# Kernel tuning notes

Hardware: AMD Instinct MI355X
Metric: run time of the kernel (lower is better)

The kernel has to match this reference:

```python
import jax, jax.numpy as jnp
import numpy as np

DIM, HEADS = 128, 8
DH = DIM // HEADS
SCALE = DH ** -0.5
N, E = 50000, 800000


def setup_inputs() -> dict:
    key = jax.random.key(0)
    ks = jax.random.split(key, 12)
    w = lambda k: jax.random.normal(k, (DIM, DIM), dtype=jnp.float32) * 0.02
    b = lambda k: jax.random.normal(k, (DIM,), dtype=jnp.float32) * 0.02
    return {
        "q_nodes": jax.random.normal(ks[0], (N, DIM), dtype=jnp.float32),
        "k_edges": jax.random.normal(ks[1], (E, DIM), dtype=jnp.float32),
        "v_edges": jax.random.normal(ks[2], (E, DIM), dtype=jnp.float32),
        "edge_index": jax.random.randint(ks[3], (2, E), 0, N, dtype=jnp.int64),
        "Wq": w(ks[4]), "bq": b(ks[5]),
        "Wk": w(ks[6]), "bk": b(ks[7]),
        "Wv": w(ks[8]), "bv": b(ks[9]),
        "Wo": w(ks[10]), "bo": b(ks[11]),
    }


def reference(q_nodes, k_edges, v_edges, edge_index, Wq, bq, Wk, bk, Wv, bv, Wo, bo):
    n, e = q_nodes.shape[0], k_edges.shape[0]
    dst = edge_index[0]  # src (edge_index[1]) is unused by the module
    q = (q_nodes @ Wq.T + bq).reshape(n, HEADS, DH)
    k = (k_edges @ Wk.T + bk).reshape(e, HEADS, DH)
    v = (v_edges @ Wv.T + bv).reshape(e, HEADS, DH)
    # per-edge score: dot(q[dst], k) per head -> [E, H]
    score = jnp.einsum('ehd,ehd->eh', q[dst], k) * SCALE
    # segment (per-dst-node) softmax over edges, numerically stable
    m = jax.ops.segment_max(score, dst, num_segments=n)          # [N, H]
    ex = jnp.exp(score - m[dst])                                  # [E, H]
    s = jax.ops.segment_sum(ex, dst, num_segments=n)             # [N, H]
    w = ex / (s[dst] + 1e-16)                                     # [E, H]
    weighted_v = (v * w[..., None]).reshape(e, DIM)               # [E, dim]
    aggr = jax.ops.segment_sum(weighted_v, dst, num_segments=n)  # [N, dim]
    return aggr @ Wo.T + bo
```

## Files before the change

### kernel.cpp

```cpp
#include <hip/hip_runtime.h>

#define TM 64
#define NTHREADS 256
#define PAD 132

typedef __attribute__((ext_vector_type(8))) short short8;
typedef __attribute__((ext_vector_type(4))) float f32x4;

__device__ __forceinline__ short f2bf(float f) {
  union { float f; unsigned u; } uf; uf.f = f;
  unsigned r = uf.u + 0x7FFFu + ((uf.u >> 16) & 1u);
  return (short)(r >> 16);
}
__device__ __forceinline__ float bf2f(short s) {
  union { unsigned u; float f; } uf; uf.u = ((unsigned)(unsigned short)s) << 16;
  return uf.f;
}
__device__ __forceinline__ short8 pack8(float4 a, float4 b) {
  short8 r;
  r[0] = f2bf(a.x); r[1] = f2bf(a.y); r[2] = f2bf(a.z); r[3] = f2bf(a.w);
  r[4] = f2bf(b.x); r[5] = f2bf(b.y); r[6] = f2bf(b.z); r[7] = f2bf(b.w);
  return r;
}


__global__ __launch_bounds__(512) void proj_mfma(
    const float* __restrict__ X, const short* __restrict__ Wb,
    const float* __restrict__ bias, float* __restrict__ Y, int M, float scale) {
  __shared__ short Xb[8192];
  int t = threadIdx.x;
  int w = t >> 6, l = t & 63, g = l >> 4, c = l & 15;
  short8 wf[4];
#pragma unroll
  for (int kc = 0; kc < 4; ++kc)
    wf[kc] = *(const short8*)(Wb + (w * 16 + c) * 128 + kc * 32 + g * 8);
  float4 b4 = *(const float4*)(bias + w * 16 + g * 4);

  for (int rb = blockIdx.x * 64; rb < M; rb += gridDim.x * 64) {
    {
      int r = t >> 3, q8 = t & 7;
      int row = rb + r; if (row >= M) row = M - 1;
      const float4* xs = (const float4*)(X + (size_t)row * 128 + q8 * 16);
      float4 x0 = xs[0], x1 = xs[1], x2 = xs[2], x3 = xs[3];
      int sw = (r & 7) << 4;
      *(short8*)((char*)Xb + r * 256 + ((q8 * 32) ^ sw)) = pack8(x0, x1);
      *(short8*)((char*)Xb + r * 256 + ((q8 * 32 + 16) ^ sw)) = pack8(x2, x3);
    }
    __syncthreads();
#pragma unroll
    for (int et = 0; et < 4; ++et) {
      int rl = et * 16 + c;
      f32x4 acc = {};
      int sw = (rl & 7) << 4;
#pragma unroll
      for (int kc = 0; kc < 4; ++kc) {
        short8 xb = *(const short8*)((char*)Xb + rl * 256 + ((kc * 64 + g * 16) ^ sw));
        acc = __builtin_amdgcn_mfma_f32_16x16x32_bf16(wf[kc], xb, acc, 0, 0, 0);
      }
      int row = rb + rl;
      if (row < M) {
        float4 o;
        o.x = (acc[0] + b4.x) * scale; o.y = (acc[1] + b4.y) * scale;
        o.z = (acc[2] + b4.z) * scale; o.w = (acc[3] + b4.w) * scale;
        *(float4*)(Y + (size_t)row * 128 + w * 16 + g * 4) = o;
      }
    }
    __syncthreads();
  }
}


__global__ __launch_bounds__(512) void proj_mfma_h(
    const float* __restrict__ X, const short* __restrict__ Wb,
    const float* __restrict__ bias, short* __restrict__ Yh, int M, float scale) {
  __shared__ short Xb[8192];
  int t = threadIdx.x;
  int w = t >> 6, l = t & 63, g = l >> 4, c = l & 15;
  short8 wf[4];
#pragma unroll
  for (int kc = 0; kc < 4; ++kc)
    wf[kc] = *(const short8*)(Wb + (w * 16 + c) * 128 + kc * 32 + g * 8);
  float4 b4 = *(const float4*)(bias + w * 16 + g * 4);

  for (int rb = blockIdx.x * 64; rb < M; rb += gridDim.x * 64) {
    {
      int r = t >> 3, q8 = t & 7;
      int row = rb + r; if (row >= M) row = M - 1;
      const float4* xs = (const float4*)(X + (size_t)row * 128 + q8 * 16);
      float4 x0 = xs[0], x1 = xs[1], x2 = xs[2], x3 = xs[3];
      int sw = (r & 7) << 4;
      *(short8*)((char*)Xb + r * 256 + ((q8 * 32) ^ sw)) = pack8(x0, x1);
      *(short8*)((char*)Xb + r * 256 + ((q8 * 32 + 16) ^ sw)) = pack8(x2, x3);
    }
    __syncthreads();
#pragma unroll
    for (int et = 0; et < 4; ++et) {
      int rl = et * 16 + c;
      f32x4 acc = {};
      int sw = (rl & 7) << 4;
#pragma unroll
      for (int kc = 0; kc < 4; ++kc) {
        short8 xb = *(const short8*)((char*)Xb + rl * 256 + ((kc * 64 + g * 16) ^ sw));
        acc = __builtin_amdgcn_mfma_f32_16x16x32_bf16(wf[kc], xb, acc, 0, 0, 0);
      }
      int row = rb + rl;
      if (row < M) {
        short4 o;
        o.x = f2bf((acc[0] + b4.x) * scale); o.y = f2bf((acc[1] + b4.y) * scale);
        o.z = f2bf((acc[2] + b4.z) * scale); o.w = f2bf((acc[3] + b4.w) * scale);
        *(short4*)(Yh + (size_t)row * 128 + w * 16 + g * 4) = o;
      }
    }
    __syncthreads();
  }
}


__global__ __launch_bounds__(256) void hist_kernel(const int* __restrict__ dst,
                                                   int* __restrict__ cnt, int E) {
  int e = blockIdx.x * 256 + threadIdx.x;
  if (e < E) atomicAdd(&cnt[dst[e]], 1);
}

__global__ __launch_bounds__(1024) void scan_part(const int* __restrict__ cnt,
                                                  int* __restrict__ part, int N) {
  __shared__ int ws[16];
  int t = threadIdx.x, i = blockIdx.x * 1024 + t;
  int v = (i < N) ? cnt[i] : 0;
#pragma unroll
  for (int d = 1; d < 64; d <<= 1) v += __shfl_xor(v, d);
  if ((t & 63) == 0) ws[t >> 6] = v;
  __syncthreads();
  if (t < 16) {
    int x = ws[t];
#pragma unroll
    for (int d = 1; d < 16; d <<= 1) x += __shfl_xor(x, d);
    if (t == 0) part[blockIdx.x] = x;
  }
}

__global__ __launch_bounds__(64) void scan_offs(int* __restrict__ part, int P) {
  int t = threadIdx.x;
  int carry = 0;
  for (int base = 0; base < P; base += 64) {
    int i = base + t;
    int v = (i < P) ? part[i] : 0;
    int x = v;
#pragma unroll
    for (int d = 1; d < 64; d <<= 1) { int y = __shfl_up(x, d); if (t >= d) x += y; }
    if (i < P) part[i] = x - v + carry;
    carry += __shfl(x, 63);
  }
}

__global__ __launch_bounds__(1024) void scan_final(const int* __restrict__ cnt,
                                                   const int* __restrict__ part,
                                                   int* __restrict__ rp,
                                                   int* __restrict__ cur, int N) {
  __shared__ int ws[16];
  __shared__ int wofs[16];
  int t = threadIdx.x, i = blockIdx.x * 1024 + t;
  int lane = t & 63, wid = t >> 6;
  int v = (i < N) ? cnt[i] : 0;
  int x = v;
#pragma unroll
  for (int d = 1; d < 64; d <<= 1) { int y = __shfl_up(x, d); if (lane >= d) x += y; }
  if (lane == 63) ws[wid] = x;
  __syncthreads();
  if (t == 0) {
    int s = 0;
#pragma unroll
    for (int k2 = 0; k2 < 16; ++k2) { int tmp = ws[k2]; wofs[k2] = s; s += tmp; }
  }
  __syncthreads();
  int incl = x + wofs[wid] + part[blockIdx.x];
  int excl = incl - v;
  if (i < N) {
    rp[i] = excl; cur[i] = excl;
    if (i == N - 1) rp[N] = incl;
  }
}

__global__ __launch_bounds__(256) void perm_kernel(const int* __restrict__ dst,
                                                   int* __restrict__ cursor,
                                                   int* __restrict__ perm, int E) {
  int e = blockIdx.x * 256 + threadIdx.x;
  if (e < E) perm[e] = atomicAdd(&cursor[dst[e]], 1);
}

__global__ __launch_bounds__(256) void wprep4(
    const float* __restrict__ Wq, const float* __restrict__ Wk,
    const float* __restrict__ Wv, const float* __restrict__ Wo,
    short* __restrict__ wqb, short* __restrict__ wkb,
    short* __restrict__ wvb, short* __restrict__ wob) {
  int i = blockIdx.x * 256 + threadIdx.x;
  if (i < 16384) {
    wqb[i] = f2bf(Wq[i]); wkb[i] = f2bf(Wk[i]);
    wvb[i] = f2bf(Wv[i]); wob[i] = f2bf(Wo[i]);
  }
}


__global__ __launch_bounds__(512) void edge_mfma9(
    const float* __restrict__ K, const float* __restrict__ V,
    const int* __restrict__ eidx, const int* __restrict__ perm,
    const short* __restrict__ wkb, const short* __restrict__ wvb,
    const float* __restrict__ bk, const short* __restrict__ qpb,
    float* __restrict__ exb, short* __restrict__ wv, int E) {
  __shared__ short Kb[8192];
  __shared__ short Vb[8192];
  __shared__ int sh_perm[64];
  int t = threadIdx.x;
  int w = t >> 6, l = t & 63, g = l >> 4, c = l & 15;
  float4 bk4 = *(const float4*)(bk + w * 16 + g * 4);
  const short* wkp = wkb + (w * 16 + c) * 128 + g * 8;
  const short* wvp = wvb + (w * 16 + c) * 128 + g * 8;
  const short* qpp = qpb + (size_t)(w * 16 + g * 4);

  int r = t >> 3, q8 = t & 7;
  int b0 = r * 256 + ((q8 * 32) ^ ((r & 7) << 4));
  int stride = gridDim.x * 64;
  int eb = blockIdx.x * 64;

  float4 k0, k1, k2, k3, v0, v1, v2, v3;
  short4 qvb[4];
  int prm_r;
  {
    int row0 = eb + r; if (row0 >= E) row0 = E - 1;
    const float4* ks = (const float4*)(K + (size_t)row0 * 128 + q8 * 16);
    k0 = ks[0]; k1 = ks[1]; k2 = ks[2]; k3 = ks[3];
    const float4* vs = (const float4*)(V + (size_t)row0 * 128 + q8 * 16);
    v0 = vs[0]; v1 = vs[1]; v2 = vs[2]; v3 = vs[3];
    prm_r = perm[row0];
#pragma unroll
    for (int et = 0; et < 4; ++et) {
      int e = eb + et * 16 + c; if (e >= E) e = E - 1;
      qvb[et] = *(const short4*)(qpp + (size_t)eidx[e] * 128);
    }
  }

  for (; eb < E; eb += stride) {
    int ebn = eb + stride;
    bool hn = ebn < E;

    __syncthreads();
    *(short8*)((char*)Kb + b0) = pack8(k0, k1);
    *(short8*)((char*)Kb + (b0 ^ 16)) = pack8(k2, k3);
    *(short8*)((char*)Vb + b0) = pack8(v0, v1);
    *(short8*)((char*)Vb + (b0 ^ 16)) = pack8(v2, v3);
    if (q8 == 0) sh_perm[r] = prm_r;
    __syncthreads();

    short8 wK[4];
#pragma unroll
    for (int kc = 0; kc < 4; ++kc)
      wK[kc] = *(const short8*)(wkp + kc * 32);

    short4 qvn[4];
    int prm_rn = 0;
    if (hn) {
      int rowk = ebn + r; if (rowk >= E) rowk = E - 1;
      const float4* ks = (const float4*)(K + (size_t)rowk * 128 + q8 * 16);
      k0 = ks[0]; k1 = ks[1]; k2 = ks[2]; k3 = ks[3];
      const float4* vs = (const float4*)(V + (size_t)rowk * 128 + q8 * 16);
      v0 = vs[0]; v1 = vs[1]; v2 = vs[2]; v3 = vs[3];
      prm_rn = perm[rowk];
#pragma unroll
      for (int et = 0; et < 4; ++et) {
        int e = ebn + et * 16 + c; if (e >= E) e = E - 1;
        qvn[et] = *(const short4*)(qpp + (size_t)eidx[e] * 128);
      }
    }

    float ex[4];
    int sl[4];
#pragma unroll
    for (int et = 0; et < 4; ++et) {
      int eloc = et * 16 + c;
      int swr = (eloc & 7) << 4;
      sl[et] = sh_perm[eloc];
      f32x4 acc = {};
#pragma unroll
      for (int kc = 0; kc < 4; ++kc) {
        short8 xb = *(const short8*)((char*)Kb + eloc * 256 + ((kc * 64 + g * 16) ^ swr));
        acc = __builtin_amdgcn_mfma_f32_16x16x32_bf16(wK[kc], xb, acc, 0, 0, 0);
      }
      float s = (acc[0] + bk4.x) * bf2f(qvb[et].x) + (acc[1] + bk4.y) * bf2f(qvb[et].y) +
                (acc[2] + bk4.z) * bf2f(qvb[et].z) + (acc[3] + bk4.w) * bf2f(qvb[et].w);
      s += __shfl_xor(s, 16);
      s += __shfl_xor(s, 32);
      ex[et] = __expf(s);
      if (g == 0) exb[(size_t)sl[et] * 8 + w] = ex[et];
    }

    short8 wV[4];
#pragma unroll
    for (int kc = 0; kc < 4; ++kc)
      wV[kc] = *(const short8*)(wvp + kc * 32);

#pragma unroll
    for (int et = 0; et < 4; ++et) {
      int eloc = et * 16 + c;
      int swr = (eloc & 7) << 4;
      f32x4 acc = {};
#pragma unroll
      for (int kc = 0; kc < 4; ++kc) {
        short8 xb = *(const short8*)((char*)Vb + eloc * 256 + ((kc * 64 + g * 16) ^ swr));
        acc = __builtin_amdgcn_mfma_f32_16x16x32_bf16(wV[kc], xb, acc, 0, 0, 0);
      }
      short4 sv;
      sv.x = f2bf(acc[0] * ex[et]); sv.y = f2bf(acc[1] * ex[et]);
      sv.z = f2bf(acc[2] * ex[et]); sv.w = f2bf(acc[3] * ex[et]);
      *(short4*)(wv + (size_t)sl[et] * 128 + w * 16 + g * 4) = sv;
    }

#pragma unroll
    for (int et = 0; et < 4; ++et) qvb[et] = qvn[et];
    prm_r = prm_rn;
  }
}


__global__ __launch_bounds__(256) void pull3(
    const short* __restrict__ wv, const float* __restrict__ exb,
    const int* __restrict__ rp, const float* __restrict__ bv,
    float* __restrict__ aggr, int N) {
  int w = threadIdx.x >> 6, l = threadIdx.x & 63;
  int n = blockIdx.x * 4 + w;
  if (n >= N) return;
  int beg = rp[n], end = rp[n + 1];
  int h = l >> 3;
  float a0 = 0.f, a1 = 0.f, s = 0.f;
  int j = beg;
  for (; j + 1 < end; j += 2) {
    unsigned u0 = *(const unsigned*)(wv + (size_t)j * 128 + l * 2);
    unsigned u1 = *(const unsigned*)(wv + (size_t)(j + 1) * 128 + l * 2);
    float s0 = exb[(size_t)j * 8 + h], s1 = exb[(size_t)(j + 1) * 8 + h];
    a0 += bf2f((short)(u0 & 0xFFFFu)) + bf2f((short)(u1 & 0xFFFFu));
    a1 += bf2f((short)(u0 >> 16)) + bf2f((short)(u1 >> 16));
    s += s0 + s1;
  }
  if (j < end) {
    unsigned u0 = *(const unsigned*)(wv + (size_t)j * 128 + l * 2);
    s += exb[(size_t)j * 8 + h];
    a0 += bf2f((short)(u0 & 0xFFFFu));
    a1 += bf2f((short)(u0 >> 16));
  }
  float2 o;
  if (end > beg) {
    float inv = 1.f / (s + 1e-16f);
    float2 bvv = *(const float2*)(bv + l * 2);
    o.x = a0 * inv + bvv.x; o.y = a1 * inv + bvv.y;
  } else {
    o.x = 0.f; o.y = 0.f;
  }
  *(float2*)(aggr + (size_t)n * 128 + l * 2) = o;
}


__device__ __forceinline__ void stage_x(float (*Xs)[PAD], const float* __restrict__ X,
                                        int rowbase, int M, int t) {
#pragma unroll
  for (int i = 0; i < 8; ++i) {
    int idx = t + NTHREADS * i;
    int r = idx >> 5, q = idx & 31;
    int row = rowbase + r;
    if (row >= M) row = M - 1;
    const float4 v = *(const float4*)(X + (size_t)row * 128 + q * 4);
    *(float4*)(&Xs[r][q * 4]) = v;
  }
}

__device__ __forceinline__ void gemm_tile(const float (*Xs)[PAD], float (*WT)[PAD],
                                          const float* __restrict__ W,
                                          float acc[8][4], int r0, int c0, int t) {
#pragma unroll 1
  for (int kk = 0; kk < 128; kk += 32) {
    {
      int j = t >> 1, half = t & 1;
      const float* src = W + j * 128 + kk + half * 16;
      float4 a = *(const float4*)(src);
      float4 b = *(const float4*)(src + 4);
      float4 c = *(const float4*)(src + 8);
      float4 d = *(const float4*)(src + 12);
      int cb = half * 16;
      WT[cb + 0][j] = a.x;  WT[cb + 1][j] = a.y;  WT[cb + 2][j] = a.z;  WT[cb + 3][j] = a.w;
      WT[cb + 4][j] = b.x;  WT[cb + 5][j] = b.y;  WT[cb + 6][j] = b.z;  WT[cb + 7][j] = b.w;
      WT[cb + 8][j] = c.x;  WT[cb + 9][j] = c.y;  WT[cb + 10][j] = c.z; WT[cb + 11][j] = c.w;
      WT[cb + 12][j] = d.x; WT[cb + 13][j] = d.y; WT[cb + 14][j] = d.z; WT[cb + 15][j] = d.w;
    }
    __syncthreads();
#pragma unroll
    for (int c2 = 0; c2 < 16; ++c2) {
      float4 wa = *(const float4*)(&WT[2 * c2][c0]);
      float4 wb = *(const float4*)(&WT[2 * c2 + 1][c0]);
#pragma unroll
      for (int i = 0; i < 8; ++i) {
        float2 xv = *(const float2*)(&Xs[r0 + i][kk + 2 * c2]);
        acc[i][0] = fmaf(xv.x, wa.x, acc[i][0]);
        acc[i][1] = fmaf(xv.x, wa.y, acc[i][1]);
        acc[i][2] = fmaf(xv.x, wa.z, acc[i][2]);
        acc[i][3] = fmaf(xv.x, wa.w, acc[i][3]);
        acc[i][0] = fmaf(xv.y, wb.x, acc[i][0]);
        acc[i][1] = fmaf(xv.y, wb.y, acc[i][1]);
        acc[i][2] = fmaf(xv.y, wb.z, acc[i][2]);
        acc[i][3] = fmaf(xv.y, wb.w, acc[i][3]);
      }
    }
    __syncthreads();
  }
}

__global__ __launch_bounds__(NTHREADS) void proj_kernel(
    const float* __restrict__ X, const float* __restrict__ W,
    const float* __restrict__ b, float* __restrict__ Y, int M) {
  __shared__ float Xs[TM][PAD];
  __shared__ float WT[32][PAD];
  int t = threadIdx.x;
  int B0 = blockIdx.x * TM;
  stage_x(Xs, X, B0, M, t);
  __syncthreads();
  int r0 = (t >> 5) * 8, m = t & 31, c0 = m * 4;
  float acc[8][4] = {};
  gemm_tile(Xs, WT, W, acc, r0, c0, t);
  float4 bv = ((const float4*)b)[m];
#pragma unroll
  for (int i = 0; i < 8; ++i) {
    int row = B0 + r0 + i;
    if (row < M) {
      float4 o;
      o.x = acc[i][0] + bv.x; o.y = acc[i][1] + bv.y;
      o.z = acc[i][2] + bv.z; o.w = acc[i][3] + bv.w;
      *(float4*)(Y + (size_t)row * 128 + c0) = o;
    }
  }
}

__global__ __launch_bounds__(NTHREADS) void edge_kernel(
    const float* __restrict__ Kin, const float* __restrict__ Vin,
    const int* __restrict__ eidx,
    const float* __restrict__ Wk, const float* __restrict__ bk,
    const float* __restrict__ Wv, const float* __restrict__ bv,
    const float* __restrict__ qp, float* __restrict__ s_sum,
    float* __restrict__ aggr, int E) {
  __shared__ float Xs[TM][PAD];
  __shared__ float WT[32][PAD];
  __shared__ int dsts[TM];
  int t = threadIdx.x;
  int e0 = blockIdx.x * TM;
  if (t < TM) {
    int idx = e0 + t;
    if (idx >= E) idx = E - 1;
    dsts[t] = eidx[idx];
  }
  stage_x(Xs, Kin, e0, E, t);
  __syncthreads();
  int r0 = (t >> 5) * 8, m = t & 31, c0 = m * 4;
  int h = m >> 2;
  float acc[8][4] = {};
  gemm_tile(Xs, WT, Wk, acc, r0, c0, t);
  float4 bkv = ((const float4*)bk)[m];
  float ex[8];
#pragma unroll
  for (int i = 0; i < 8; ++i) {
    int r = r0 + i;
    const float4 qv = *(const float4*)(qp + (size_t)dsts[r] * 128 + c0);
    float p = (acc[i][0] + bkv.x) * qv.x + (acc[i][1] + bkv.y) * qv.y +
              (acc[i][2] + bkv.z) * qv.z + (acc[i][3] + bkv.w) * qv.w;
    p += __shfl_xor(p, 1);
    p += __shfl_xor(p, 2);
    float e = __expf(p * 0.25f);
    ex[i] = e;
    if ((m & 3) == 0 && (e0 + r) < E)
      atomicAdd(&s_sum[(size_t)dsts[r] * 8 + h], e);
  }
  __syncthreads();
  stage_x(Xs, Vin, e0, E, t);
  __syncthreads();
#pragma unroll
  for (int i = 0; i < 8; ++i)
#pragma unroll
    for (int j = 0; j < 4; ++j) acc[i][j] = 0.f;
  gemm_tile(Xs, WT, Wv, acc, r0, c0, t);
  float4 bvv = ((const float4*)bv)[m];
#pragma unroll
  for (int i = 0; i < 8; ++i) {
    int r = r0 + i;
    if ((e0 + r) < E) {
      size_t base = (size_t)dsts[r] * 128 + c0;
      atomicAdd(&aggr[base + 0], (acc[i][0] + bvv.x) * ex[i]);
      atomicAdd(&aggr[base + 1], (acc[i][1] + bvv.y) * ex[i]);
      atomicAdd(&aggr[base + 2], (acc[i][2] + bvv.z) * ex[i]);
      atomicAdd(&aggr[base + 3], (acc[i][3] + bvv.w) * ex[i]);
    }
  }
}

__global__ __launch_bounds__(NTHREADS) void out_kernel(
    const float* __restrict__ aggr, const float* __restrict__ s_sum,
    const float* __restrict__ W, const float* __restrict__ b,
    float* __restrict__ Y, int M) {
  __shared__ float Xs[TM][PAD];
  __shared__ float WT[32][PAD];
  int t = threadIdx.x;
  int B0 = blockIdx.x * TM;
#pragma unroll
  for (int i = 0; i < 8; ++i) {
    int idx = t + NTHREADS * i;
    int r = idx >> 5, q = idx & 31;
    int row = B0 + r;
    if (row >= M) row = M - 1;
    float4 v = *(const float4*)(aggr + (size_t)row * 128 + q * 4);
    float inv = 1.0f / (s_sum[(size_t)row * 8 + (q >> 2)] + 1e-16f);
    v.x *= inv; v.y *= inv; v.z *= inv; v.w *= inv;
    *(float4*)(&Xs[r][q * 4]) = v;
  }
  __syncthreads();
  int r0 = (t >> 5) * 8, m = t & 31, c0 = m * 4;
  float acc[8][4] = {};
  gemm_tile(Xs, WT, W, acc, r0, c0, t);
  float4 bv = ((const float4*)b)[m];
#pragma unroll
  for (int i = 0; i < 8; ++i) {
    int row = B0 + r0 + i;
    if (row < M) {
      float4 o;
      o.x = acc[i][0] + bv.x; o.y = acc[i][1] + bv.y;
      o.z = acc[i][2] + bv.z; o.w = acc[i][3] + bv.w;
      *(float4*)(Y + (size_t)row * 128 + c0) = o;
    }
  }
}


extern "C" void kernel_launch(void* const* d_in, const int* in_sizes, int n_in,
                              void* d_out, int out_size, void* d_ws, size_t ws_size,
                              hipStream_t stream) {
  const float* q_nodes = (const float*)d_in[0];
  const float* k_edges = (const float*)d_in[1];
  const float* v_edges = (const float*)d_in[2];
  const int* eidx = (const int*)d_in[3];
  const float* Wq = (const float*)d_in[4];
  const float* bq = (const float*)d_in[5];
  const float* Wk = (const float*)d_in[6];
  const float* bk = (const float*)d_in[7];
  const float* Wv = (const float*)d_in[8];
  const float* bv = (const float*)d_in[9];
  const float* Wo = (const float*)d_in[10];
  const float* bo = (const float*)d_in[11];

  int N = in_sizes[0] / 128;
  int E = in_sizes[1] / 128;
  int P = (N + 1023) / 1024;

  size_t off = 0;
  auto alloc = [&](size_t b) { size_t o = off; off += (b + 255) & ~(size_t)255; return o; };
  size_t o_qpb  = alloc((size_t)N * 128 * 2);
  size_t o_aggr = alloc((size_t)N * 128 * 4);
  size_t o_exb  = alloc((size_t)E * 8 * 4);
  size_t o_rp   = alloc(((size_t)N + 1) * 4);
  size_t o_cur  = alloc((size_t)N * 4);
  size_t o_cnt  = alloc((size_t)N * 4);
  size_t o_perm = alloc((size_t)E * 4);
  size_t o_part = alloc((size_t)(P + 1) * 4);
  size_t o_wqb  = alloc((size_t)16384 * 2);
  size_t o_wkb  = alloc((size_t)16384 * 2);
  size_t o_wvb  = alloc((size_t)16384 * 2);
  size_t o_wob  = alloc((size_t)16384 * 2);
  size_t o_wv   = alloc((size_t)E * 128 * 2);

  if (off <= ws_size) {
    char* base = (char*)d_ws;
    short* qpb   = (short*)(base + o_qpb);
    float* aggr  = (float*)(base + o_aggr);
    float* exb   = (float*)(base + o_exb);
    int*   rp    = (int*)(base + o_rp);
    int*   cur   = (int*)(base + o_cur);
    int*   cnt   = (int*)(base + o_cnt);
    int*   perm  = (int*)(base + o_perm);
    int*   part  = (int*)(base + o_part);
    short* wqb   = (short*)(base + o_wqb);
    short* wkb   = (short*)(base + o_wkb);
    short* wvb   = (short*)(base + o_wvb);
    short* wob   = (short*)(base + o_wob);
    short* wvbuf = (short*)(base + o_wv);

    hipMemsetAsync(cnt, 0, (size_t)N * 4, stream);
    wprep4<<<64, 256, 0, stream>>>(Wq, Wk, Wv, Wo, wqb, wkb, wvb, wob);
    proj_mfma_h<<<(N + 63) / 64, 512, 0, stream>>>(q_nodes, wqb, bq, qpb, N, 0.25f);
    hist_kernel<<<(E + 255) / 256, 256, 0, stream>>>(eidx, cnt, E);
    scan_part<<<P, 1024, 0, stream>>>(cnt, part, N);
    scan_offs<<<1, 64, 0, stream>>>(part, P);
    scan_final<<<P, 1024, 0, stream>>>(cnt, part, rp, cur, N);
    perm_kernel<<<(E + 255) / 256, 256, 0, stream>>>(eidx, cur, perm, E);

    int eblk = (E + 63) / 64; if (eblk > 1024) eblk = 1024;
    edge_mfma9<<<eblk, 512, 0, stream>>>(k_edges, v_edges, eidx, perm, wkb, wvb,
                                         bk, qpb, exb, wvbuf, E);
    pull3<<<(N + 3) / 4, 256, 0, stream>>>(wvbuf, exb, rp, bv, aggr, N);
    proj_mfma<<<(N + 63) / 64, 512, 0, stream>>>(aggr, wob, bo, (float*)d_out, N, 1.0f);
  } else {
    float* q_proj = (float*)d_ws;
    float* s_sum  = q_proj + (size_t)N * 128;
    float* aggr   = s_sum + (size_t)N * 8;
    hipMemsetAsync(s_sum, 0, (size_t)N * 136 * sizeof(float), stream);
    int nblk = (N + TM - 1) / TM;
    int eblk = (E + TM - 1) / TM;
    proj_kernel<<<nblk, NTHREADS, 0, stream>>>(q_nodes, Wq, bq, q_proj, N);
    edge_kernel<<<eblk, NTHREADS, 0, stream>>>(k_edges, v_edges, eidx, Wk, bk, Wv, bv,
                                               q_proj, s_sum, aggr, E);
    out_kernel<<<nblk, NTHREADS, 0, stream>>>(aggr, s_sum, Wo, bo, (float*)d_out, N);
  }
}
```

Before: 442.2 us.

## Replace LDS-staged edge projection with register-resident per-wave edge tiles

The edge kernel no longer stages K/V rows through shared memory with barriers and software prefetch. Each wave now loads its 16 edges' K and V rows directly into registers as MFMA B-operands and loops over all 8 heads, streaming weight fragments from global/L1. This removes LDS traffic and __syncthreads and writes exb as contiguous float4 per edge. In exchange it drops the explicit next-iteration prefetch and reloads the weights per head from cache; block size and grid cap change to match.

```diff
diff --git a/kernel.cpp b/kernel.cpp
--- a/kernel.cpp
+++ b/kernel.cpp
@@ -201,122 +201,88 @@
 }
 
 
-__global__ __launch_bounds__(512) void edge_mfma9(
+__global__ __launch_bounds__(256) void edge_nolds(
     const float* __restrict__ K, const float* __restrict__ V,
     const int* __restrict__ eidx, const int* __restrict__ perm,
     const short* __restrict__ wkb, const short* __restrict__ wvb,
     const float* __restrict__ bk, const short* __restrict__ qpb,
     float* __restrict__ exb, short* __restrict__ wv, int E) {
-  __shared__ short Kb[8192];
-  __shared__ short Vb[8192];
-  __shared__ int sh_perm[64];
   int t = threadIdx.x;
   int w = t >> 6, l = t & 63, g = l >> 4, c = l & 15;
-  float4 bk4 = *(const float4*)(bk + w * 16 + g * 4);
-  const short* wkp = wkb + (w * 16 + c) * 128 + g * 8;
-  const short* wvp = wvb + (w * 16 + c) * 128 + g * 8;
-  const short* qpp = qpb + (size_t)(w * 16 + g * 4);
-
-  int r = t >> 3, q8 = t & 7;
-  int b0 = r * 256 + ((q8 * 32) ^ ((r & 7) << 4));
   int stride = gridDim.x * 64;
-  int eb = blockIdx.x * 64;
-
-  float4 k0, k1, k2, k3, v0, v1, v2, v3;
-  short4 qvb[4];
-  int prm_r;
-  {
-    int row0 = eb + r; if (row0 >= E) row0 = E - 1;
-    const float4* ks = (const float4*)(K + (size_t)row0 * 128 + q8 * 16);
-    k0 = ks[0]; k1 = ks[1]; k2 = ks[2]; k3 = ks[3];
-    const float4* vs = (const float4*)(V + (size_t)row0 * 128 + q8 * 16);
-    v0 = vs[0]; v1 = vs[1]; v2 = vs[2]; v3 = vs[3];
-    prm_r = perm[row0];
-#pragma unroll
-    for (int et = 0; et < 4; ++et) {
-      int e = eb + et * 16 + c; if (e >= E) e = E - 1;
-      qvb[et] = *(const short4*)(qpp + (size_t)eidx[e] * 128);
-    }
-  }
-
-  for (; eb < E; eb += stride) {
-    int ebn = eb + stride;
-    bool hn = ebn < E;
-
-    __syncthreads();
-    *(short8*)((char*)Kb + b0) = pack8(k0, k1);
-    *(short8*)((char*)Kb + (b0 ^ 16)) = pack8(k2, k3);
-    *(short8*)((char*)Vb + b0) = pack8(v0, v1);
-    *(short8*)((char*)Vb + (b0 ^ 16)) = pack8(v2, v3);
-    if (q8 == 0) sh_perm[r] = prm_r;
-    __syncthreads();
-
-    short8 wK[4];
-#pragma unroll
-    for (int kc = 0; kc < 4; ++kc)
-      wK[kc] = *(const short8*)(wkp + kc * 32);
-
-    short4 qvn[4];
-    int prm_rn = 0;
-    if (hn) {
-      int rowk = ebn + r; if (rowk >= E) rowk = E - 1;
-      const float4* ks = (const float4*)(K + (size_t)rowk * 128 + q8 * 16);
-      k0 = ks[0]; k1 = ks[1]; k2 = ks[2]; k3 = ks[3];
-      const float4* vs = (const float4*)(V + (size_t)rowk * 128 + q8 * 16);
-      v0 = vs[0]; v1 = vs[1]; v2 = vs[2]; v3 = vs[3];
-      prm_rn = perm[rowk];
-#pragma unroll
-      for (int et = 0; et < 4; ++et) {
-        int e = ebn + et * 16 + c; if (e >= E) e = E - 1;
-        qvn[et] = *(const short4*)(qpp + (size_t)eidx[e] * 128);
-      }
-    }
-
-    float ex[4];
-    int sl[4];
-#pragma unroll
-    for (int et = 0; et < 4; ++et) {
-      int eloc = et * 16 + c;
-      int swr = (eloc & 7) << 4;
-      sl[et] = sh_perm[eloc];
+
+  for (int eb0 = blockIdx.x * 64; eb0 < E; eb0 += stride) {
+    int e = eb0 + w * 16 + c;
+    int ec = e < E ? e : E - 1;
+
+    const short* wkbi = wkb;
+    const short* wvbi = wvb;
+    const float* bki  = bk;
+    asm volatile("" : "+v"(wkbi), "+v"(wvbi), "+v"(bki));
+
+    int d = eidx[ec];
+    int slot = perm[ec];
+
+    const float* kr = K + (size_t)ec * 128 + g * 8;
+    const float* vr = V + (size_t)ec * 128 + g * 8;
+    short8 kf[4], vf[4];
+#pragma unroll
+    for (int kc = 0; kc < 4; ++kc) {
+      float4 a = *(const float4*)(kr + kc * 32);
+      float4 b = *(const float4*)(kr + kc * 32 + 4);
+      kf[kc] = pack8(a, b);
+    }
+#pragma unroll
+    for (int kc = 0; kc < 4; ++kc) {
+      float4 a = *(const float4*)(vr + kc * 32);
+      float4 b = *(const float4*)(vr + kc * 32 + 4);
+      vf[kc] = pack8(a, b);
+    }
+    const short* qrow = qpb + (size_t)d * 128 + g * 4;
+    short4 qv[8];
+#pragma unroll
+    for (int h = 0; h < 8; ++h) qv[h] = *(const short4*)(qrow + h * 16);
+
+    float ex[8];
+#pragma unroll
+    for (int h = 0; h < 8; ++h) {
+      const short* wkp = wkbi + (h * 16 + c) * 128 + g * 8;
       f32x4 acc = {};
 #pragma unroll
       for (int kc = 0; kc < 4; ++kc) {
-        short8 xb = *(const short8*)((char*)Kb + eloc * 256 + ((kc * 64 + g * 16) ^ swr));
-        acc = __builtin_amdgcn_mfma_f32_16x16x32_bf16(wK[kc], xb, acc, 0, 0, 0);
-      }
-      float s = (acc[0] + bk4.x) * bf2f(qvb[et].x) + (acc[1] + bk4.y) * bf2f(qvb[et].y) +
-                (acc[2] + bk4.z) * bf2f(qvb[et].z) + (acc[3] + bk4.w) * bf2f(qvb[et].w);
+        short8 wf = *(const short8*)(wkp + kc * 32);
+        acc = __builtin_amdgcn_mfma_f32_16x16x32_bf16(wf, kf[kc], acc, 0, 0, 0);
+      }
+      float4 bk4 = *(const float4*)(bki + h * 16 + g * 4);
+      float s = (acc[0] + bk4.x) * bf2f(qv[h].x) + (acc[1] + bk4.y) * bf2f(qv[h].y) +
+                (acc[2] + bk4.z) * bf2f(qv[h].z) + (acc[3] + bk4.w) * bf2f(qv[h].w);
       s += __shfl_xor(s, 16);
       s += __shfl_xor(s, 32);
-      ex[et] = __expf(s);
-      if (g == 0) exb[(size_t)sl[et] * 8 + w] = ex[et];
-    }
-
-    short8 wV[4];
-#pragma unroll
-    for (int kc = 0; kc < 4; ++kc)
-      wV[kc] = *(const short8*)(wvp + kc * 32);
-
-#pragma unroll
-    for (int et = 0; et < 4; ++et) {
-      int eloc = et * 16 + c;
-      int swr = (eloc & 7) << 4;
+      ex[h] = __expf(s);
+    }
+    if (g == 0 && e < E) {
+      float4 e0 = {ex[0], ex[1], ex[2], ex[3]};
+      float4 e1 = {ex[4], ex[5], ex[6], ex[7]};
+      *(float4*)(exb + (size_t)slot * 8) = e0;
+      *(float4*)(exb + (size_t)slot * 8 + 4) = e1;
+    }
+
+#pragma unroll
+    for (int h = 0; h < 8; ++h) {
+      const short* wvp = wvbi + (h * 16 + c) * 128 + g * 8;
       f32x4 acc = {};
 #pragma unroll
       for (int kc = 0; kc < 4; ++kc) {
-        short8 xb = *(const short8*)((char*)Vb + eloc * 256 + ((kc * 64 + g * 16) ^ swr));
-        acc = __builtin_amdgcn_mfma_f32_16x16x32_bf16(wV[kc], xb, acc, 0, 0, 0);
-      }
-      short4 sv;
-      sv.x = f2bf(acc[0] * ex[et]); sv.y = f2bf(acc[1] * ex[et]);
-      sv.z = f2bf(acc[2] * ex[et]); sv.w = f2bf(acc[3] * ex[et]);
-      *(short4*)(wv + (size_t)sl[et] * 128 + w * 16 + g * 4) = sv;
-    }
-
-#pragma unroll
-    for (int et = 0; et < 4; ++et) qvb[et] = qvn[et];
-    prm_r = prm_rn;
+        short8 wf = *(const short8*)(wvp + kc * 32);
+        acc = __builtin_amdgcn_mfma_f32_16x16x32_bf16(wf, vf[kc], acc, 0, 0, 0);
+      }
+      if (e < E) {
+        short4 sv;
+        sv.x = f2bf(acc[0] * ex[h]); sv.y = f2bf(acc[1] * ex[h]);
+        sv.z = f2bf(acc[2] * ex[h]); sv.w = f2bf(acc[3] * ex[h]);
+        *(short4*)(wv + (size_t)slot * 128 + h * 16 + g * 4) = sv;
+      }
+    }
   }
 }
 
@@ -594,8 +560,8 @@
     scan_final<<<P, 1024, 0, stream>>>(cnt, part, rp, cur, N);
     perm_kernel<<<(E + 255) / 256, 256, 0, stream>>>(eidx, cur, perm, E);
 
-    int eblk = (E + 63) / 64; if (eblk > 1024) eblk = 1024;
-    edge_mfma9<<<eblk, 512, 0, stream>>>(k_edges, v_edges, eidx, perm, wkb, wvb,
+    int eblk = (E + 63) / 64; if (eblk > 4096) eblk = 4096;
+    edge_nolds<<<eblk, 256, 0, stream>>>(k_edges, v_edges, eidx, perm, wkb, wvb,
                                          bk, qpb, exb, wvbuf, E);
     pull3<<<(N + 3) / 4, 256, 0, stream>>>(wvbuf, exb, rp, bv, aggr, N);
     proj_mfma<<<(N + 63) / 64, 512, 0, stream>>>(aggr, wob, bo, (float*)d_out, N, 1.0f);
```

After: 711.1 us. 1.61x slower.
